# Performance work log

Measured on AMD Instinct MI355X. Metric: run time of the kernel, lower is better.

The kernel has to match this reference:

```python
import jax, jax.numpy as jnp
import numpy as np


def setup_inputs() -> dict:
    key = jax.random.key(0)
    ks = jax.random.split(key, 8)
    B, C, N = 2, 128, 8192
    E, NNZ = 1024, 4096
    return {
        "vertex_feat": jax.random.normal(ks[0], (B, C, N), dtype=jnp.float32),
        "edge_feat": jax.random.normal(ks[1], (B, C, E), dtype=jnp.float32),
        "edge_weight": jax.random.uniform(ks[2], (E,), dtype=jnp.float32),
        "incidence": jax.random.randint(ks[3], (2, NNZ), 0, E, dtype=jnp.int64),
        "inv_edge_degree": jax.random.uniform(ks[4], (E,), dtype=jnp.float32),
        "inv_vertex_degree": jax.random.uniform(ks[5], (N,), dtype=jnp.float32),
        "edge_scale": jnp.ones((1,), dtype=jnp.float32),
        "knn_k": 20,
    }


def _knn_edge_aggregate(vertex_feat, knn_k):
    # vertex_feat: [B, C, N]
    B, C, N = vertex_feat.shape
    x = vertex_feat
    xx = jnp.sum(x * x, axis=1)                      # [B, N]
    inner = -2.0 * jnp.einsum("bcn,bcm->bnm", x, x)  # [B, N, N]
    dist = xx[:, :, None] + inner + xx[:, None, :]    # [B, N, N]
    # topk of -dist, drop self (nearest)
    _, idx = jax.lax.top_k(-dist, knn_k + 1)          # [B, N, k+1]
    idx = idx[:, :, 1:]                               # [B, N, k]
    vf = jnp.transpose(x, (0, 2, 1))                  # [B, N, C]
    # batched gather of neighbor features -> [B, N, k, C]
    neighbor = vf[jnp.arange(B)[:, None, None], idx]
    rel = neighbor - vf[:, :, None, :]                # relative positions
    m = jnp.max(rel, axis=2)                          # [B, N, C]
    return x + jnp.transpose(m, (0, 2, 1))            # [B, C, N]


def reference(vertex_feat, edge_feat, edge_weight, incidence,
              inv_edge_degree, inv_vertex_degree, edge_scale, knn_k):
    # use_knn=True path of feature_aggregation_layer.forward;
    # edge_* / incidence / degree args are unused in this branch.
    return _knn_edge_aggregate(vertex_feat, knn_k)
```

## Files before the change

kernel.cpp:

```cpp
#include <hip/hip_runtime.h>

#define NQ 8192
#define CD 128
#define NB 2
#define KNN 20
#define QB 32
#define TB 128
#define LDC 136
#define LDSD 132
#define LOSCALE 4096.0f
#define LOINV (1.0f / 4096.0f)

using f16x8 = __attribute__((ext_vector_type(8))) _Float16;
using f16x2 = __attribute__((ext_vector_type(2))) _Float16;
using f32x4 = __attribute__((ext_vector_type(4))) float;

__global__ __launch_bounds__(256) void k_transpose(const float* __restrict__ x,
                                                   _Float16* __restrict__ vhi,
                                                   _Float16* __restrict__ vlo) {
  __shared__ float tile[32][33];
  int bid = blockIdx.x;
  int ctile = bid & 3;
  int ntile = (bid >> 2) & 255;
  int b = bid >> 10;
  int c0 = ctile << 5, n0 = ntile << 5;
  int tx = threadIdx.x & 31, ty = threadIdx.x >> 5;
  const float* xb = x + (size_t)b * CD * NQ;
  _Float16* hb = vhi + (size_t)b * NQ * CD;
  _Float16* lb = vlo + (size_t)b * NQ * CD;
#pragma unroll
  for (int i = 0; i < 4; ++i) {
    int c = ty + (i << 3);
    tile[c][tx] = xb[(size_t)(c0 + c) * NQ + n0 + tx];
  }
  __syncthreads();
#pragma unroll
  for (int i = 0; i < 4; ++i) {
    int n = ty + (i << 3);
    float v = tile[tx][n];
    _Float16 h = (_Float16)v;
    float hf = (float)h;
    _Float16 l = (_Float16)((v - hf) * LOSCALE);
    size_t o = (size_t)(n0 + n) * CD + c0 + tx;
    hb[o] = h;
    lb[o] = l;
  }
}

__global__ __launch_bounds__(256) void k_xx(const float* __restrict__ x,
                                            float* __restrict__ xx) {
  int n = blockIdx.x * 256 + threadIdx.x;
  int b = blockIdx.y;
  const float* xb = x + (size_t)b * CD * NQ + n;
  float s = 0.f;
#pragma unroll
  for (int c = 0; c < CD; ++c) {
    float v = xb[(size_t)c * NQ];
    s += v * v;
  }
  xx[(size_t)b * NQ + n] = s;
}

__global__ __launch_bounds__(512, 4) void k_knn(const _Float16* __restrict__ vhi,
                                                const _Float16* __restrict__ vlo,
                                                const float* __restrict__ xx,
                                                int* __restrict__ idxout) {
  __shared__ char ubuf[TB * LDC * 2];
  __shared__ _Float16 clo[TB][LDC];
  __shared__ float xq[QB];
  __shared__ float xc[TB];
  auto chi = (_Float16(*)[LDC])ubuf;
  auto sd = (float(*)[LDSD])ubuf;

  const int t = threadIdx.x;
  const int blk = blockIdx.x;
  const int b = blk >> 8;
  const int q0 = (blk & 255) * QB;
  const _Float16* hb = vhi + (size_t)b * NQ * CD;
  const _Float16* lb = vlo + (size_t)b * NQ * CD;
  const float* xb = xx + (size_t)b * NQ;

  const int lane = t & 63, w = t >> 6;
  const int strip = w & 1;
  const int quarter = w >> 1;

  if (t < QB) xq[t] = xb[q0 + t];

  f16x8 ahi[4], alo[4];
  {
    int row = q0 + 16 * strip + (lane & 15);
    int kof = (lane >> 4) * 8;
    const _Float16* hrow = hb + (size_t)row * CD + kof;
    const _Float16* lrow = lb + (size_t)row * CD + kof;
#pragma unroll
    for (int ks = 0; ks < 4; ++ks) {
      ahi[ks] = *(const f16x8*)(hrow + ks * 32);
      alo[ks] = *(const f16x8*)(lrow + ks * 32);
    }
  }

  float ed[4]; int ei[4]; float tau[4];
#pragma unroll
  for (int u = 0; u < 4; ++u) { ed[u] = 3.0e38f; ei[u] = 0; tau[u] = 3.0e38f; }

  auto insert1 = [&](float& edu, int& eiu, float d, int ci) {
    float sh = __shfl_up(edu, 1);
    int shi = __shfl_up(eiu, 1);
    bool cprev = (lane > 0) && (d < sh);
    bool ccur = d < edu;
    edu = ccur ? (cprev ? sh : d) : edu;
    eiu = ccur ? (cprev ? shi : ci) : eiu;
  };

  for (int tile = 0; tile < NQ / TB; ++tile) {
    const int c0 = tile * TB;
    __syncthreads();

#pragma unroll
    for (int i = 0; i < 4; ++i) {
      int e = t + i * 512;
      int r = e >> 4, ch = (e & 15) * 8;
      *(f16x8*)&chi[r][ch] = *(const f16x8*)(hb + (size_t)(c0 + r) * CD + ch);
      *(f16x8*)&clo[r][ch] = *(const f16x8*)(lb + (size_t)(c0 + r) * CD + ch);
    }
    if (t < TB) xc[t] = xb[c0 + t];
    __syncthreads();

    f32x4 accA[2], accB[2];
#pragma unroll
    for (int f = 0; f < 2; ++f) {
      accA[f] = (f32x4){0.f, 0.f, 0.f, 0.f};
      accB[f] = (f32x4){0.f, 0.f, 0.f, 0.f};
    }
    const int kof = (lane >> 4) * 8;
#pragma unroll
    for (int ks = 0; ks < 4; ++ks) {
#pragma unroll
      for (int f = 0; f < 2; ++f) {
        int c = 32 * quarter + 16 * f + (lane & 15);
        f16x8 bhi = *(const f16x8*)&chi[c][ks * 32 + kof];
        f16x8 blo = *(const f16x8*)&clo[c][ks * 32 + kof];
        accA[f] = __builtin_amdgcn_mfma_f32_16x16x32_f16(ahi[ks], bhi, accA[f], 0, 0, 0);
        accB[f] = __builtin_amdgcn_mfma_f32_16x16x32_f16(ahi[ks], blo, accB[f], 0, 0, 0);
        accB[f] = __builtin_amdgcn_mfma_f32_16x16x32_f16(alo[ks], bhi, accB[f], 0, 0, 0);
      }
    }

    float dv[2][4];
#pragma unroll
    for (int f = 0; f < 2; ++f) {
      int c = 32 * quarter + 16 * f + (lane & 15);
      float xcv = xc[c];
#pragma unroll
      for (int r = 0; r < 4; ++r) {
        int qrow = 16 * strip + (lane >> 4) * 4 + r;
        float dot = accA[f][r] + accB[f][r] * LOINV;
        float tmp = xq[qrow] + (-2.0f * dot);
        dv[f][r] = tmp + xcv;
      }
    }
    __syncthreads();
#pragma unroll
    for (int f = 0; f < 2; ++f) {
      int c = 32 * quarter + 16 * f + (lane & 15);
#pragma unroll
      for (int r = 0; r < 4; ++r) {
        int qrow = 16 * strip + (lane >> 4) * 4 + r;
        sd[qrow][c] = dv[f][r];
      }
    }
    __syncthreads();

#pragma unroll
    for (int u = 0; u < 4; ++u) {
      int q = 4 * w + u;
      int qg = q0 + q;
      float d0 = sd[q][lane];
      float d1 = sd[q][64 + lane];
      int cnt = 0;
      unsigned long long m0 = __ballot(d0 < tau[u] && (c0 + lane) != qg);
      while (m0) {
        int l = __builtin_ctzll(m0); m0 &= m0 - 1;
        float d = __shfl(d0, l);
        if (d < tau[u]) {
          insert1(ed[u], ei[u], d, c0 + l);
          if ((++cnt & 7) == 0) tau[u] = __shfl(ed[u], 19);
        }
      }
      tau[u] = __shfl(ed[u], 19);
      unsigned long long m1 = __ballot(d1 < tau[u] && (c0 + 64 + lane) != qg);
      while (m1) {
        int l = __builtin_ctzll(m1); m1 &= m1 - 1;
        float d = __shfl(d1, l);
        if (d < tau[u]) {
          insert1(ed[u], ei[u], d, c0 + 64 + l);
          if ((++cnt & 7) == 0) tau[u] = __shfl(ed[u], 19);
        }
      }
      tau[u] = __shfl(ed[u], 19);
    }
  }

  if (lane < KNN) {
#pragma unroll
    for (int u = 0; u < 4; ++u)
      idxout[(size_t)(b * NQ + q0 + 4 * w + u) * KNN + lane] = ei[u];
  }
}

__global__ __launch_bounds__(256) void k_gather(const _Float16* __restrict__ vhi,
                                                const _Float16* __restrict__ vlo,
                                                const int* __restrict__ idx,
                                                float* __restrict__ out) {
  __shared__ float tile[CD][65];
  int blk = blockIdx.x;
  int b = blk >> 7;
  int n0 = (blk & 127) * 64;
  int w = threadIdx.x >> 6, lane = threadIdx.x & 63;
  const _Float16* hb = vhi + (size_t)b * NQ * CD;
  const _Float16* lb = vlo + (size_t)b * NQ * CD;
  for (int s = 0; s < 16; ++s) {
    int nl = w * 16 + s;
    const int* id = idx + (size_t)(b * NQ + n0 + nl) * KNN;
    float ma = -3.0e38f, mb = -3.0e38f;
#pragma unroll
    for (int j = 0; j < KNN; ++j) {
      size_t ro = (size_t)id[j] * CD + 2 * lane;
      f16x2 h = *(const f16x2*)(hb + ro);
      f16x2 l = *(const f16x2*)(lb + ro);
      ma = fmaxf(ma, fmaf((float)l[0], LOINV, (float)h[0]));
      mb = fmaxf(mb, fmaf((float)l[1], LOINV, (float)h[1]));
    }
    tile[2 * lane][nl] = ma;
    tile[2 * lane + 1][nl] = mb;
  }
  __syncthreads();
  float* ob = out + (size_t)b * CD * NQ;
  for (int i = 0; i < 32; ++i) {
    int e = threadIdx.x + i * 256;
    int c = e >> 6, j = e & 63;
    ob[(size_t)c * NQ + n0 + j] = tile[c][j];
  }
}

extern "C" void kernel_launch(void* const* d_in, const int* in_sizes, int n_in,
                              void* d_out, int out_size, void* d_ws, size_t ws_size,
                              hipStream_t stream) {
  const float* x = (const float*)d_in[0];
  size_t velems = (size_t)NB * NQ * CD;
  _Float16* vhi = (_Float16*)d_ws;
  _Float16* vlo = vhi + velems;
  float* xx = (float*)((char*)d_ws + velems * 4);
  int* idx = (int*)((char*)xx + (size_t)NB * NQ * 4);
  float* out = (float*)d_out;

  k_transpose<<<dim3(NB * 256 * 4), dim3(256), 0, stream>>>(x, vhi, vlo);
  k_xx<<<dim3(NQ / 256, NB), dim3(256), 0, stream>>>(x, xx);
  k_knn<<<dim3(NB * NQ / QB), dim3(512), 0, stream>>>(vhi, vlo, xx, idx);
  k_gather<<<dim3(NB * NQ / 64), dim3(256), 0, stream>>>(vhi, vlo, idx, out);
}
```

Measured before the change: 370.6 us.

## Prefetch next candidate tile into registers and use LDS-only barriers in kNN

The kNN kernel now issues global loads for the next 128-candidate tile into registers before the MFMA and top-k selection of the current tile, and writes them to shared memory afterwards. The __syncthreads calls are replaced by a barrier that waits only on LDS counters, so global loads stay in flight across barriers. The separate register staging of distances is dropped, which removes one barrier per tile. The cost is about 32 extra VGPRs per thread under launch_bounds(512,4), which risks spills or lower occupancy.

```diff
diff --git a/kernel.cpp b/kernel.cpp
--- a/kernel.cpp
+++ b/kernel.cpp
@@ -14,6 +14,13 @@
 using f16x8 = __attribute__((ext_vector_type(8))) _Float16;
 using f16x2 = __attribute__((ext_vector_type(2))) _Float16;
 using f32x4 = __attribute__((ext_vector_type(4))) float;
+
+#define LGKM_BARRIER()                                         \
+  do {                                                         \
+    asm volatile("s_waitcnt lgkmcnt(0)" ::: "memory");         \
+    __builtin_amdgcn_s_barrier();                              \
+    asm volatile("" ::: "memory");                             \
+  } while (0)
 
 __global__ __launch_bounds__(256) void k_transpose(const float* __restrict__ x,
                                                    _Float16* __restrict__ vhi,
@@ -99,6 +106,26 @@
     }
   }
 
+  const int pr = t >> 4, pch = (t & 15) * 8;
+  f16x8 ph[4], pl[4];
+  float pxc = 0.f;
+
+#pragma unroll
+  for (int i = 0; i < 4; ++i) {
+    int r = pr + i * 32;
+    ph[i] = *(const f16x8*)(hb + (size_t)r * CD + pch);
+    pl[i] = *(const f16x8*)(lb + (size_t)r * CD + pch);
+  }
+  if (t < TB) pxc = xb[t];
+#pragma unroll
+  for (int i = 0; i < 4; ++i) {
+    int r = pr + i * 32;
+    *(f16x8*)&chi[r][pch] = ph[i];
+    *(f16x8*)&clo[r][pch] = pl[i];
+  }
+  if (t < TB) xc[t] = pxc;
+  LGKM_BARRIER();
+
   float ed[4]; int ei[4]; float tau[4];
 #pragma unroll
   for (int u = 0; u < 4; ++u) { ed[u] = 3.0e38f; ei[u] = 0; tau[u] = 3.0e38f; }
@@ -112,19 +139,21 @@
     eiu = ccur ? (cprev ? shi : ci) : eiu;
   };
 
-  for (int tile = 0; tile < NQ / TB; ++tile) {
+  const int NT = NQ / TB;
+  for (int tile = 0; tile < NT; ++tile) {
     const int c0 = tile * TB;
-    __syncthreads();
-
-#pragma unroll
-    for (int i = 0; i < 4; ++i) {
-      int e = t + i * 512;
-      int r = e >> 4, ch = (e & 15) * 8;
-      *(f16x8*)&chi[r][ch] = *(const f16x8*)(hb + (size_t)(c0 + r) * CD + ch);
-      *(f16x8*)&clo[r][ch] = *(const f16x8*)(lb + (size_t)(c0 + r) * CD + ch);
-    }
-    if (t < TB) xc[t] = xb[c0 + t];
-    __syncthreads();
+    const bool more = (tile + 1 < NT);
+
+    if (more) {
+      const int cn = c0 + TB;
+#pragma unroll
+      for (int i = 0; i < 4; ++i) {
+        int r = cn + pr + i * 32;
+        ph[i] = *(const f16x8*)(hb + (size_t)r * CD + pch);
+        pl[i] = *(const f16x8*)(lb + (size_t)r * CD + pch);
+      }
+      if (t < TB) pxc = xb[cn + t];
+    }
 
     f32x4 accA[2], accB[2];
 #pragma unroll
@@ -146,7 +175,8 @@
       }
     }
 
-    float dv[2][4];
+    LGKM_BARRIER();
+
 #pragma unroll
     for (int f = 0; f < 2; ++f) {
       int c = 32 * quarter + 16 * f + (lane & 15);
@@ -156,20 +186,10 @@
         int qrow = 16 * strip + (lane >> 4) * 4 + r;
         float dot = accA[f][r] + accB[f][r] * LOINV;
         float tmp = xq[qrow] + (-2.0f * dot);
-        dv[f][r] = tmp + xcv;
-      }
-    }
-    __syncthreads();
-#pragma unroll
-    for (int f = 0; f < 2; ++f) {
-      int c = 32 * quarter + 16 * f + (lane & 15);
-#pragma unroll
-      for (int r = 0; r < 4; ++r) {
-        int qrow = 16 * strip + (lane >> 4) * 4 + r;
-        sd[qrow][c] = dv[f][r];
-      }
-    }
-    __syncthreads();
+        sd[qrow][c] = tmp + xcv;
+      }
+    }
+    LGKM_BARRIER();
 
 #pragma unroll
     for (int u = 0; u < 4; ++u) {
@@ -198,6 +218,18 @@
         }
       }
       tau[u] = __shfl(ed[u], 19);
+    }
+
+    if (more) {
+      LGKM_BARRIER();
+#pragma unroll
+      for (int i = 0; i < 4; ++i) {
+        int r = pr + i * 32;
+        *(f16x8*)&chi[r][pch] = ph[i];
+        *(f16x8*)&clo[r][pch] = pl[i];
+      }
+      if (t < TB) xc[t] = pxc;
+      LGKM_BARRIER();
     }
   }
 
```

Result: slower. 409.4 us (+10.5%).

## Select kNN candidates with fp16 only, then rerank top-32 at higher precision

Applied to the files above, without the earlier changes.

The distance pass now uses only the hi fp16 half in the MFMA tile loop. This drops the lo-part LDS tile, its global loads and two of the three MFMAs per step. Each query keeps 32 candidates instead of 20, and a final pass recomputes their exact distances from hi+lo data and bitonic-sorts them across lanes to pick the top 20. The trade is a small per-query rerank cost. It also risks missing a true neighbor if fp16 error pushes it outside the top 32.

```diff
diff --git a/kernel.cpp b/kernel.cpp
--- a/kernel.cpp
+++ b/kernel.cpp
@@ -8,6 +8,7 @@
 #define TB 128
 #define LDC 136
 #define LDSD 132
+#define NSEL 32
 #define LOSCALE 4096.0f
 #define LOINV (1.0f / 4096.0f)
 
@@ -66,7 +67,6 @@
                                                 const float* __restrict__ xx,
                                                 int* __restrict__ idxout) {
   __shared__ char ubuf[TB * LDC * 2];
-  __shared__ _Float16 clo[TB][LDC];
   __shared__ float xq[QB];
   __shared__ float xc[TB];
   auto chi = (_Float16(*)[LDC])ubuf;
@@ -86,17 +86,13 @@
 
   if (t < QB) xq[t] = xb[q0 + t];
 
-  f16x8 ahi[4], alo[4];
+  f16x8 ahi[4];
   {
     int row = q0 + 16 * strip + (lane & 15);
     int kof = (lane >> 4) * 8;
     const _Float16* hrow = hb + (size_t)row * CD + kof;
-    const _Float16* lrow = lb + (size_t)row * CD + kof;
-#pragma unroll
-    for (int ks = 0; ks < 4; ++ks) {
-      ahi[ks] = *(const f16x8*)(hrow + ks * 32);
-      alo[ks] = *(const f16x8*)(lrow + ks * 32);
-    }
+#pragma unroll
+    for (int ks = 0; ks < 4; ++ks) ahi[ks] = *(const f16x8*)(hrow + ks * 32);
   }
 
   float ed[4]; int ei[4]; float tau[4];
@@ -121,17 +117,13 @@
       int e = t + i * 512;
       int r = e >> 4, ch = (e & 15) * 8;
       *(f16x8*)&chi[r][ch] = *(const f16x8*)(hb + (size_t)(c0 + r) * CD + ch);
-      *(f16x8*)&clo[r][ch] = *(const f16x8*)(lb + (size_t)(c0 + r) * CD + ch);
     }
     if (t < TB) xc[t] = xb[c0 + t];
     __syncthreads();
 
-    f32x4 accA[2], accB[2];
-#pragma unroll
-    for (int f = 0; f < 2; ++f) {
-      accA[f] = (f32x4){0.f, 0.f, 0.f, 0.f};
-      accB[f] = (f32x4){0.f, 0.f, 0.f, 0.f};
-    }
+    f32x4 accA[2];
+    accA[0] = (f32x4){0.f, 0.f, 0.f, 0.f};
+    accA[1] = (f32x4){0.f, 0.f, 0.f, 0.f};
     const int kof = (lane >> 4) * 8;
 #pragma unroll
     for (int ks = 0; ks < 4; ++ks) {
@@ -139,10 +131,7 @@
       for (int f = 0; f < 2; ++f) {
         int c = 32 * quarter + 16 * f + (lane & 15);
         f16x8 bhi = *(const f16x8*)&chi[c][ks * 32 + kof];
-        f16x8 blo = *(const f16x8*)&clo[c][ks * 32 + kof];
         accA[f] = __builtin_amdgcn_mfma_f32_16x16x32_f16(ahi[ks], bhi, accA[f], 0, 0, 0);
-        accB[f] = __builtin_amdgcn_mfma_f32_16x16x32_f16(ahi[ks], blo, accB[f], 0, 0, 0);
-        accB[f] = __builtin_amdgcn_mfma_f32_16x16x32_f16(alo[ks], bhi, accB[f], 0, 0, 0);
       }
     }
 
@@ -154,8 +143,7 @@
 #pragma unroll
       for (int r = 0; r < 4; ++r) {
         int qrow = 16 * strip + (lane >> 4) * 4 + r;
-        float dot = accA[f][r] + accB[f][r] * LOINV;
-        float tmp = xq[qrow] + (-2.0f * dot);
+        float tmp = xq[qrow] + (-2.0f * accA[f][r]);
         dv[f][r] = tmp + xcv;
       }
     }
@@ -184,27 +172,64 @@
         float d = __shfl(d0, l);
         if (d < tau[u]) {
           insert1(ed[u], ei[u], d, c0 + l);
-          if ((++cnt & 7) == 0) tau[u] = __shfl(ed[u], 19);
+          if ((++cnt & 7) == 0) tau[u] = __shfl(ed[u], NSEL - 1);
         }
       }
-      tau[u] = __shfl(ed[u], 19);
+      tau[u] = __shfl(ed[u], NSEL - 1);
       unsigned long long m1 = __ballot(d1 < tau[u] && (c0 + 64 + lane) != qg);
       while (m1) {
         int l = __builtin_ctzll(m1); m1 &= m1 - 1;
         float d = __shfl(d1, l);
         if (d < tau[u]) {
           insert1(ed[u], ei[u], d, c0 + 64 + l);
-          if ((++cnt & 7) == 0) tau[u] = __shfl(ed[u], 19);
+          if ((++cnt & 7) == 0) tau[u] = __shfl(ed[u], NSEL - 1);
         }
       }
-      tau[u] = __shfl(ed[u], 19);
-    }
-  }
-
-  if (lane < KNN) {
-#pragma unroll
-    for (int u = 0; u < 4; ++u)
-      idxout[(size_t)(b * NQ + q0 + 4 * w + u) * KNN + lane] = ei[u];
+      tau[u] = __shfl(ed[u], NSEL - 1);
+    }
+  }
+
+#pragma unroll 1
+  for (int u = 0; u < 4; ++u) {
+    const int r32 = lane & 31;
+    const int qloc = 4 * w + u;
+    const int qg2 = q0 + qloc;
+    int ci = __shfl(ei[u], r32);
+
+    const _Float16* qh = hb + (size_t)qg2 * CD;
+    const _Float16* qlw = lb + (size_t)qg2 * CD;
+    const _Float16* ch = hb + (size_t)ci * CD;
+    const _Float16* cl = lb + (size_t)ci * CD;
+    float dot = 0.f;
+#pragma unroll 2
+    for (int kc = 0; kc < CD / 8; ++kc) {
+      f16x8 ah = *(const f16x8*)(qh + kc * 8);
+      f16x8 al = *(const f16x8*)(qlw + kc * 8);
+      f16x8 bh = *(const f16x8*)(ch + kc * 8);
+      f16x8 bl = *(const f16x8*)(cl + kc * 8);
+#pragma unroll
+      for (int e = 0; e < 8; ++e) {
+        float qv = fmaf((float)al[e], LOINV, (float)ah[e]);
+        float cv = fmaf((float)bl[e], LOINV, (float)bh[e]);
+        dot = fmaf(qv, cv, dot);
+      }
+    }
+    float dex = (xq[qloc] + (-2.0f * dot)) + xb[ci];
+
+#pragma unroll
+    for (int k = 2; k <= 32; k <<= 1) {
+#pragma unroll
+      for (int j2 = k >> 1; j2 >= 1; j2 >>= 1) {
+        float od = __shfl_xor(dex, j2);
+        int oi = __shfl_xor(ci, j2);
+        bool lower = !(r32 & j2);
+        bool up = ((r32 & k) == 0) || (k == 32);
+        bool tt = (od < dex) || (od == dex && oi < ci);
+        if (tt == (lower == up)) { dex = od; ci = oi; }
+      }
+    }
+    if (lane < KNN)
+      idxout[(size_t)(b * NQ + qg2) * KNN + lane] = ci;
   }
 }
 
```

Result: slower. 441.6 us (+19.2%).
